# Kernel optimization log

Hardware: AMD Instinct MI355X
Metric: run time of the kernel (lower is better)

## Reference

```python
import math
import jax, jax.numpy as jnp
import numpy as np

D_MODEL = 512
N_HEADS = 8
HD = D_MODEL // N_HEADS  # 64
RATIO = 8      # csa_compress_ratio
STRIDE = 4     # csa_compress_stride
WINDOW = 128   # csa_window_size
THETA = 10000.0


def _rope_freqs(L):
    half = HD // 2
    inv_freq = 1.0 / (THETA ** (jnp.arange(half, dtype=jnp.float32) / half))
    t = jnp.arange(L, dtype=jnp.float32)
    f = t[:, None] * inv_freq[None, :]  # [L, half]
    return jnp.cos(f), jnp.sin(f)


def _apply_rope(x, cos, sin):
    # x: [B, H, L, hd]
    half = x.shape[-1] // 2
    x1, x2 = x[..., :half], x[..., half:]
    cos = cos[None, None]
    sin = sin[None, None]
    return jnp.concatenate([x1 * cos - x2 * sin, x1 * sin + x2 * cos], axis=-1)


def setup_inputs() -> dict:
    key = jax.random.key(0)
    ks = jax.random.split(key, 9)
    B, L, D = 2, 2048, D_MODEL
    s = 0.02
    return {
        "x": jax.random.normal(ks[0], (B, L, D), dtype=jnp.float32),
        "wq": jax.random.normal(ks[1], (D, D), dtype=jnp.float32) * s,
        "wk": jax.random.normal(ks[2], (D, D), dtype=jnp.float32) * s,
        "wv": jax.random.normal(ks[3], (D, D), dtype=jnp.float32) * s,
        "wo": jax.random.normal(ks[4], (D, D), dtype=jnp.float32) * s,
        "wk_c": jax.random.normal(ks[5], (D, D), dtype=jnp.float32) * s,
        "wv_c": jax.random.normal(ks[6], (D, D), dtype=jnp.float32) * s,
        "gate_logits": jax.random.normal(ks[7], (RATIO,), dtype=jnp.float32) * s,
        "sink_logit": jnp.zeros((N_HEADS, 1), dtype=jnp.float32),
    }


def reference(x, wq, wk, wv, wo, wk_c, wv_c, gate_logits, sink_logit):
    B, L, D = x.shape
    f32 = jnp.float32

    def heads(t):  # [B,L,D] -> [B,H,L,hd]
        return t.reshape(B, L, N_HEADS, HD).transpose(0, 2, 1, 3)

    q = heads(x @ wq.T)
    k = heads(x @ wk.T)
    v = heads(x @ wv.T)

    cos, sin = _rope_freqs(L)
    q = _apply_rope(q.astype(f32), cos, sin).astype(x.dtype)
    k = _apply_rope(k.astype(f32), cos, sin).astype(x.dtype)

    # --- KV compression: strided overlapping windows, learned gate pooling ---
    n_windows = max(1, (L - RATIO) // STRIDE + 1)
    idx = jnp.clip(
        jnp.arange(RATIO)[None, :] + jnp.arange(n_windows)[:, None] * STRIDE, 0, L - 1
    )  # [Lc, ratio]
    windows = x[:, idx, :]  # [B, Lc, ratio, D]
    gate_w = jax.nn.softmax(gate_logits)
    x_c = jnp.einsum("bwrd,r->bwd", windows, gate_w)  # [B, Lc, D]
    Lc = n_windows

    k_c = x_c @ wk_c.T
    v_c = x_c @ wv_c.T
    k_c = k_c.reshape(B, Lc, N_HEADS, HD).transpose(0, 2, 1, 3)
    v_c = v_c.reshape(B, Lc, N_HEADS, HD).transpose(0, 2, 1, 3)

    scale = math.sqrt(HD)
    pos = jnp.arange(L)

    # compressed branch: causal on compressed-entry end positions
    comp_scores = jnp.einsum("bhqd,bhkd->bhqk", q, k_c) / scale  # [B,H,L,Lc]
    entry_end = jnp.arange(Lc) * STRIDE + RATIO - 1
    causal_c = pos[:, None] >= entry_end[None, :]
    comp_scores = jnp.where(causal_c[None, None], comp_scores, -jnp.inf)

    # local window branch: causal band of width WINDOW
    win_scores = jnp.einsum("bhqd,bhkd->bhqk", q, k) / scale  # [B,H,L,L]
    dist = pos[:, None] - pos[None, :]
    win_mask = (dist >= 0) & (dist < WINDOW)
    win_scores = jnp.where(win_mask[None, None], win_scores, -jnp.inf)

    sink = jnp.broadcast_to(sink_logit[None, :, None, :], (B, N_HEADS, L, 1))

    all_scores = jnp.concatenate(
        [comp_scores.astype(f32), win_scores.astype(f32), sink.astype(f32)], axis=-1
    )
    attn = jax.nn.softmax(all_scores, axis=-1).astype(x.dtype)

    w_comp = attn[..., :Lc]
    w_win = attn[..., Lc:Lc + L]
    out = jnp.einsum("bhqk,bhkd->bhqd", w_comp, v_c) + jnp.einsum(
        "bhqk,bhkd->bhqd", w_win, v
    )
    out = out.transpose(0, 2, 1, 3).reshape(B, L, D)
    return out @ wo.T
```

## Files before the change

### kernel.cpp

```cpp
#include <hip/hip_runtime.h>
#include <hip/hip_bf16.h>
#include <cmath>

#define BATCH 2
#define LSEQ 2048
#define DMODEL 512
#define NHEADS 8
#define HD 64
#define RATIO 8
#define STRIDE 4
#define WINDOW 128
#define LC 511

typedef short short8 __attribute__((ext_vector_type(8)));
typedef float floatx4 __attribute__((ext_vector_type(4)));

__device__ inline unsigned short f2bf(float f) {
  unsigned u = __float_as_uint(f);
  u += 0x7FFFu + ((u >> 16) & 1u);
  return (unsigned short)(u >> 16);
}

__device__ inline void gld_lds16(const unsigned short* g, short* l) {
  __builtin_amdgcn_global_load_lds(
      (const __attribute__((address_space(1))) unsigned int*)g,
      (__attribute__((address_space(3))) unsigned int*)l, 16, 0, 0);
}

__global__ void conv_all(const float* __restrict__ x,
                         const float* __restrict__ w0, const float* __restrict__ w1,
                         const float* __restrict__ w2, const float* __restrict__ w3,
                         const float* __restrict__ w4, const float* __restrict__ w5,
                         const float* __restrict__ gate,
                         unsigned short* __restrict__ xb,
                         unsigned short* __restrict__ wqkvb,
                         unsigned short* __restrict__ wkvcb,
                         unsigned short* __restrict__ wob,
                         unsigned short* __restrict__ xcb,
                         float2* __restrict__ cstab) {
  int idx = blockIdx.x * blockDim.x + threadIdx.x;
  if (idx < 917504) {
    const float* src;
    unsigned short* dst;
    int off;
    if (idx < 524288) {
      src = x; dst = xb; off = idx;
    } else {
      int r = idx - 524288;
      int wi = r >> 16;
      off = r & 65535;
      switch (wi) {
        case 0: src = w0; dst = wqkvb; break;
        case 1: src = w1; dst = wqkvb + 4 * 65536; break;
        case 2: src = w2; dst = wqkvb + 8 * 65536; break;
        case 3: src = w3; dst = wkvcb; break;
        case 4: src = w4; dst = wkvcb + 4 * 65536; break;
        default: src = w5; dst = wob; break;
      }
    }
    float4 v = ((const float4*)src)[off];
    ushort4 o;
    o.x = f2bf(v.x); o.y = f2bf(v.y); o.z = f2bf(v.z); o.w = f2bf(v.w);
    ((ushort4*)dst)[off] = o;
  } else if (idx < 1048320) {
    int r = idx - 917504;
    int d4 = r & 127;
    int t = r >> 7;
    int w = t % LC;
    int b = t / LC;
    float g[8];
    float m = -1e30f;
#pragma unroll
    for (int i = 0; i < 8; ++i) { g[i] = gate[i]; m = fmaxf(m, g[i]); }
    float ssum = 0.f;
#pragma unroll
    for (int i = 0; i < 8; ++i) { g[i] = __expf(g[i] - m); ssum += g[i]; }
    float inv = 1.f / ssum;
    const float* xb4 = x + ((size_t)(b * LSEQ + w * STRIDE)) * DMODEL + d4 * 4;
    float4 acc = make_float4(0.f, 0.f, 0.f, 0.f);
#pragma unroll
    for (int i = 0; i < 8; ++i) {
      float4 v = *(const float4*)(xb4 + (size_t)i * DMODEL);
      acc.x += g[i] * v.x; acc.y += g[i] * v.y;
      acc.z += g[i] * v.z; acc.w += g[i] * v.w;
    }
    ushort4 o;
    o.x = f2bf(acc.x * inv); o.y = f2bf(acc.y * inv);
    o.z = f2bf(acc.z * inv); o.w = f2bf(acc.w * inv);
    ((ushort4*)xcb)[(size_t)(b * LC + w) * 128 + d4] = o;
  } else {
    int e = idx - 1048320;
    int p = e >> 5, j = e & 31;
    float inv_freq = __expf(-(float)j * (9.210340371976184f / 32.f));
    float s, c;
    sincosf((float)p * inv_freq, &s, &c);
    cstab[e] = make_float2(c, s);
  }
}

__global__ __launch_bounds__(256) void proj_gemm(
    const unsigned short* __restrict__ xb, const unsigned short* __restrict__ xcb,
    const unsigned short* __restrict__ wqkvb, const unsigned short* __restrict__ wkvcb,
    const float2* __restrict__ cstab,
    unsigned short* __restrict__ qbuf, unsigned short* __restrict__ kbuf,
    unsigned short* __restrict__ vbuf, unsigned short* __restrict__ kcb,
    unsigned short* __restrict__ vcb) {
  __shared__ short As[128 * 64];
  __shared__ short Bs[128 * 64];
  const int tid = threadIdx.x;
  const int w = tid >> 6, l = tid & 63;
  const int lr = l & 15, lg = l >> 4;

  const int bid = blockIdx.x;
  const bool qkv = (bid < 384);
  const unsigned short* Ap;
  const unsigned short* Bp;
  int bm, bn, Am1;
  if (qkv) {
    Ap = xb; Bp = wqkvb; bm = (bid & 31) * 128; bn = (bid >> 5) * 128; Am1 = 4095;
  } else {
    int r = bid - 384;
    Ap = xcb; Bp = wkvcb; bm = (r & 7) * 128; bn = (r >> 3) * 128; Am1 = 1021;
  }
  const int wm = (w >> 1) * 64, wn = (w & 1) * 64;

  floatx4 acc[4][4];
#pragma unroll
  for (int i = 0; i < 4; ++i)
#pragma unroll
    for (int j = 0; j < 4; ++j) acc[i][j] = 0.f;

  const int trow = tid >> 3;
  const int cs = (tid & 7) ^ (trow & 7);
  size_t aoffs[4];
#pragma unroll
  for (int i = 0; i < 4; ++i) {
    int ar = bm + trow + i * 32;
    if (ar > Am1) ar = Am1;
    aoffs[i] = (size_t)ar * DMODEL + cs * 8;
  }
  const size_t boff = (size_t)(bn + trow) * DMODEL + cs * 8;
  const int ldsbase = (tid & 192) * 8;

  for (int k0 = 0; k0 < DMODEL; k0 += 64) {
    __syncthreads();
#pragma unroll
    for (int i = 0; i < 4; ++i) {
      gld_lds16(Ap + aoffs[i] + k0, As + i * 2048 + ldsbase);
      gld_lds16(Bp + boff + (size_t)i * 32 * DMODEL + k0, Bs + i * 2048 + ldsbase);
    }
    __syncthreads();

#pragma unroll
    for (int kk = 0; kk < 2; ++kk) {
      const int kc16 = kk * 4 + lg;
      short8 a[4], bf[4];
#pragma unroll
      for (int mi = 0; mi < 4; ++mi) {
        int r = wm + mi * 16 + lr;
        a[mi] = *(const short8*)&As[r * 64 + ((kc16 ^ (r & 7)) * 8)];
      }
#pragma unroll
      for (int nj = 0; nj < 4; ++nj) {
        int r = wn + nj * 16 + lr;
        bf[nj] = *(const short8*)&Bs[r * 64 + ((kc16 ^ (r & 7)) * 8)];
      }
#pragma unroll
      for (int mi = 0; mi < 4; ++mi)
#pragma unroll
        for (int nj = 0; nj < 4; ++nj)
          acc[mi][nj] = __builtin_amdgcn_mfma_f32_16x16x32_bf16(
              a[mi], bf[nj], acc[mi][nj], 0, 0, 0);
    }
  }

  if (qkv) {
    if (bn < 1024) {
      unsigned short* dst = (bn < 512) ? qbuf : kbuf;
      const int cbase = (bn + wn) & 511;
#pragma unroll
      for (int mi = 0; mi < 4; ++mi) {
#pragma unroll
        for (int i = 0; i < 4; ++i) {
          int row = bm + wm + mi * 16 + lg * 4 + i;
          int p = row & 2047;
#pragma unroll
          for (int nj = 0; nj < 2; ++nj) {
            float2 cssin = cstab[p * 32 + nj * 16 + lr];
            float a = acc[mi][nj][i], b2 = acc[mi][nj + 2][i];
            int cc = cbase + nj * 16 + lr;
            dst[(size_t)row * 512 + cc] = f2bf(a * cssin.x - b2 * cssin.y);
            dst[(size_t)row * 512 + cc + 32] = f2bf(a * cssin.y + b2 * cssin.x);
          }
        }
      }
    } else {
#pragma unroll
      for (int mi = 0; mi < 4; ++mi) {
#pragma unroll
        for (int i = 0; i < 4; ++i) {
          int row = bm + wm + mi * 16 + lg * 4 + i;
#pragma unroll
          for (int nj = 0; nj < 4; ++nj) {
            int col = bn + wn + nj * 16 + lr - 1024;
            vbuf[(size_t)row * 512 + col] = f2bf(acc[mi][nj][i]);
          }
        }
      }
    }
  } else {
    unsigned short* dst = ((bn + wn) < 512) ? kcb : vcb;
    const int cbase = (bn + wn) & 511;
#pragma unroll
    for (int mi = 0; mi < 4; ++mi) {
#pragma unroll
      for (int i = 0; i < 4; ++i) {
        int row = bm + wm + mi * 16 + lg * 4 + i;
        if (row < 1022) {
#pragma unroll
          for (int nj = 0; nj < 4; ++nj)
            dst[(size_t)row * 512 + cbase + nj * 16 + lr] = f2bf(acc[mi][nj][i]);
        }
      }
    }
  }
}

__global__ __launch_bounds__(256) void wo_gemm(
    const unsigned short* __restrict__ A, const unsigned short* __restrict__ B,
    float* __restrict__ C) {
  __shared__ short As[128 * 64];
  __shared__ short Bs[64 * 64];
  const int tid = threadIdx.x;
  const int w = tid >> 6, l = tid & 63;
  const int lr = l & 15, lg = l >> 4;
  const int bm = blockIdx.x * 128, bn = blockIdx.y * 64;
  const int wm = (w >> 1) * 64, wn = (w & 1) * 32;

  floatx4 acc[4][2];
#pragma unroll
  for (int i = 0; i < 4; ++i)
#pragma unroll
    for (int j = 0; j < 2; ++j) acc[i][j] = 0.f;

  const int trow = tid >> 3;
  const int cs = (tid & 7) ^ (trow & 7);
  const size_t aoff = (size_t)(bm + trow) * DMODEL + cs * 8;
  const size_t boff = (size_t)(bn + trow) * DMODEL + cs * 8;
  const int ldsbase = (tid & 192) * 8;

  for (int k0 = 0; k0 < DMODEL; k0 += 64) {
    __syncthreads();
#pragma unroll
    for (int i = 0; i < 4; ++i)
      gld_lds16(A + aoff + (size_t)i * 32 * DMODEL + k0, As + i * 2048 + ldsbase);
#pragma unroll
    for (int i = 0; i < 2; ++i)
      gld_lds16(B + boff + (size_t)i * 32 * DMODEL + k0, Bs + i * 2048 + ldsbase);
    __syncthreads();

#pragma unroll
    for (int kk = 0; kk < 2; ++kk) {
      const int kc16 = kk * 4 + lg;
      short8 a[4], bf[2];
#pragma unroll
      for (int mi = 0; mi < 4; ++mi) {
        int r = wm + mi * 16 + lr;
        a[mi] = *(const short8*)&As[r * 64 + ((kc16 ^ (r & 7)) * 8)];
      }
#pragma unroll
      for (int nj = 0; nj < 2; ++nj) {
        int r = wn + nj * 16 + lr;
        bf[nj] = *(const short8*)&Bs[r * 64 + ((kc16 ^ (r & 7)) * 8)];
      }
#pragma unroll
      for (int mi = 0; mi < 4; ++mi)
#pragma unroll
        for (int nj = 0; nj < 2; ++nj)
          acc[mi][nj] = __builtin_amdgcn_mfma_f32_16x16x32_bf16(
              a[mi], bf[nj], acc[mi][nj], 0, 0, 0);
    }
  }

#pragma unroll
  for (int mi = 0; mi < 4; ++mi) {
#pragma unroll
    for (int i = 0; i < 4; ++i) {
      int row = bm + wm + mi * 16 + lg * 4 + i;
#pragma unroll
      for (int nj = 0; nj < 2; ++nj)
        C[(size_t)row * 512 + bn + wn + nj * 16 + lr] = acc[mi][nj][i];
    }
  }
}

__global__ __launch_bounds__(256, 2) void attn_kernel(
    const unsigned short* __restrict__ qb, const unsigned short* __restrict__ kb,
    const unsigned short* __restrict__ vb, const unsigned short* __restrict__ kcb,
    const unsigned short* __restrict__ vcb, const float* __restrict__ sink,
    unsigned short* __restrict__ ob) {
  __shared__ short Ks[2][64][72];
  __shared__ short Vt[2][64][72];
  __shared__ short Pl[4][16][72];

  const int n = blockIdx.x;
  const int b = n >> 8;
  const int mm = n & 255;
  const int h = mm >> 5;
  int qt = mm & 31;
  if (b) qt = 31 - qt;
  const int q0 = qt * 64;
  const int tid = threadIdx.x;
  const int w = tid >> 6, l = tid & 63;
  const int lr = l & 15, lg = l >> 4;
  const int hoff = h * HD;

  short8 Qa0, Qa1;
  {
    const unsigned short* qrow =
        qb + ((size_t)(b * LSEQ + q0 + w * 16 + lr)) * DMODEL + hoff;
    Qa0 = *(const short8*)(qrow + lg * 8);
    Qa1 = *(const short8*)(qrow + 32 + lg * 8);
  }

  floatx4 Oacc[4];
#pragma unroll
  for (int f = 0; f < 4; ++f) Oacc[f] = 0.f;
  float mrow = -3.0e38f, lrow = 0.f;

  int ncm = q0 / 4 + 15;
  if (ncm > LC) ncm = LC;
  const int ntc = (ncm + 63) >> 6;
  const int w0 = (q0 > 127) ? (q0 - 127) : 0;
  const int ntw = (q0 + 64 - w0 + 63) >> 6;
  const int ntt = ntc + ntw;

  const int skey = tid >> 2, sd = (tid & 3) * 16;
  const int vkey = (tid & 31) * 2, vd = (tid >> 5) * 8;
  const int p = q0 + w * 16 + lr;

  short8 kreg0, kreg1, vreg0, vreg1;

  auto load_tile = [&](int tt) {
    const bool isC = (tt < ntc);
    const int tbase = isC ? tt * 64 : (w0 + (tt - ntc) * 64);
    const unsigned short* Kp = isC ? kcb : kb;
    const unsigned short* Vp = isC ? vcb : vb;
    const int rmax = isC ? (LC - 1) : (LSEQ - 1);
    const size_t brow = isC ? (size_t)(b * LC) : (size_t)(b * LSEQ);
    int kr = tbase + skey;      if (kr > rmax) kr = rmax;
    int vr0 = tbase + vkey;     if (vr0 > rmax) vr0 = rmax;
    int vr1 = tbase + vkey + 1; if (vr1 > rmax) vr1 = rmax;
    const unsigned short* src = Kp + (brow + kr) * DMODEL + hoff + sd;
    kreg0 = *(const short8*)(src);
    kreg1 = *(const short8*)(src + 8);
    vreg0 = *(const short8*)(Vp + (brow + vr0) * DMODEL + hoff + vd);
    vreg1 = *(const short8*)(Vp + (brow + vr1) * DMODEL + hoff + vd);
  };
  auto store_tile = [&](int bsel) {
    *(short8*)&Ks[bsel][skey][sd] = kreg0;
    *(short8*)&Ks[bsel][skey][sd + 8] = kreg1;
#pragma unroll
    for (int j = 0; j < 8; ++j) {
      unsigned pk = (unsigned)(unsigned short)vreg0[j] |
                    ((unsigned)(unsigned short)vreg1[j] << 16);
      *(unsigned*)&Vt[bsel][vd + j][vkey] = pk;
    }
  };

  load_tile(0);

  for (int tt = 0; tt < ntt; ++tt) {
    const int bsel = tt & 1;
    store_tile(bsel);
    if (tt + 1 < ntt) load_tile(tt + 1);
    __syncthreads();

    const bool isC = (tt < ntc);
    const int tbase = isC ? tt * 64 : (w0 + (tt - ntc) * 64);

    floatx4 S4[4];
    __builtin_amdgcn_s_setprio(1);
#pragma unroll
    for (int f = 0; f < 4; ++f) {
      floatx4 acc = 0.f;
      short8 kf0 = *(const short8*)&Ks[bsel][f * 16 + lr][lg * 8];
      short8 kf1 = *(const short8*)&Ks[bsel][f * 16 + lr][32 + lg * 8];
      acc = __builtin_amdgcn_mfma_f32_16x16x32_bf16(kf0, Qa0, acc, 0, 0, 0);
      acc = __builtin_amdgcn_mfma_f32_16x16x32_bf16(kf1, Qa1, acc, 0, 0, 0);
      S4[f] = acc;
    }
    __builtin_amdgcn_s_setprio(0);

    float tmax = -3.0e38f;
#pragma unroll
    for (int f = 0; f < 4; ++f) {
#pragma unroll
      for (int i = 0; i < 4; ++i) {
        const int key = tbase + f * 16 + lg * 4 + i;
        bool valid;
        if (isC) valid = (key <= LC - 1) && (p >= key * 4 + 7);
        else     valid = (p >= key) && (p - key < WINDOW);
        float s = valid ? S4[f][i] * 0.125f : -3.0e38f;
        S4[f][i] = s;
        tmax = fmaxf(tmax, s);
      }
    }
    tmax = fmaxf(tmax, __shfl_xor(tmax, 16));
    tmax = fmaxf(tmax, __shfl_xor(tmax, 32));

    if (__any(tmax > mrow)) {
      float mn = fmaxf(mrow, tmax);
      float r = __expf(mrow - mn);
      mrow = mn;
      lrow *= r;
      float rb[4];
#pragma unroll
      for (int i = 0; i < 4; ++i) rb[i] = __shfl(r, lg * 4 + i);
#pragma unroll
      for (int f = 0; f < 4; ++f) {
#pragma unroll
        for (int i = 0; i < 4; ++i) Oacc[f][i] *= rb[i];
      }
    }

    float lsum = 0.f;
#pragma unroll
    for (int f = 0; f < 4; ++f) {
      float e0 = (S4[f][0] > -1.0e38f) ? __expf(S4[f][0] - mrow) : 0.f;
      float e1 = (S4[f][1] > -1.0e38f) ? __expf(S4[f][1] - mrow) : 0.f;
      float e2 = (S4[f][2] > -1.0e38f) ? __expf(S4[f][2] - mrow) : 0.f;
      float e3 = (S4[f][3] > -1.0e38f) ? __expf(S4[f][3] - mrow) : 0.f;
      lsum += (e0 + e1) + (e2 + e3);
      uint2 pk;
      pk.x = (unsigned)f2bf(e0) | ((unsigned)f2bf(e1) << 16);
      pk.y = (unsigned)f2bf(e2) | ((unsigned)f2bf(e3) << 16);
      *(uint2*)&Pl[w][lr][f * 16 + lg * 4] = pk;
    }
    lsum += __shfl_xor(lsum, 16);
    lsum += __shfl_xor(lsum, 32);
    lrow += lsum;
    asm volatile("s_waitcnt lgkmcnt(0)" ::: "memory");

    __builtin_amdgcn_s_setprio(1);
#pragma unroll
    for (int c = 0; c < 2; ++c) {
      short8 Pa = *(const short8*)&Pl[w][lr][c * 32 + lg * 8];
#pragma unroll
      for (int f = 0; f < 4; ++f) {
        short8 Vf = *(const short8*)&Vt[bsel][f * 16 + lr][c * 32 + lg * 8];
        Oacc[f] = __builtin_amdgcn_mfma_f32_16x16x32_bf16(Pa, Vf, Oacc[f], 0, 0, 0);
      }
    }
    __builtin_amdgcn_s_setprio(0);
  }

  const float snk = sink[h];
  float ms = fmaxf(mrow, snk);
  float sc = __expf(mrow - ms);
  float li = lrow * sc + __expf(snk - ms);
  float osc = sc / li;
  float ob4[4];
#pragma unroll
  for (int i = 0; i < 4; ++i) ob4[i] = __shfl(osc, lg * 4 + i);
#pragma unroll
  for (int f = 0; f < 4; ++f) {
#pragma unroll
    for (int i = 0; i < 4; ++i) {
      size_t row = (size_t)(b * LSEQ + q0 + w * 16 + lg * 4 + i);
      ob[row * DMODEL + hoff + f * 16 + lr] = f2bf(Oacc[f][i] * ob4[i]);
    }
  }
}

extern "C" void kernel_launch(void* const* d_in, const int* in_sizes, int n_in,
                              void* d_out, int out_size, void* d_ws, size_t ws_size,
                              hipStream_t stream) {
  const float* x    = (const float*)d_in[0];
  const float* wq   = (const float*)d_in[1];
  const float* wk   = (const float*)d_in[2];
  const float* wv   = (const float*)d_in[3];
  const float* wo   = (const float*)d_in[4];
  const float* wkc  = (const float*)d_in[5];
  const float* wvc  = (const float*)d_in[6];
  const float* gate = (const float*)d_in[7];
  const float* sink = (const float*)d_in[8];
  float* out = (float*)d_out;

  const int BL  = BATCH * LSEQ;
  const int BLC = BATCH * LC;
  const int NX  = BATCH * LSEQ * DMODEL;
  const int NW  = DMODEL * DMODEL;

  char* wp = (char*)d_ws;
  auto carve = [&](size_t bytes) {
    char* r = wp;
    wp += (bytes + 255) & ~(size_t)255;
    return r;
  };
  unsigned short* qbuf = (unsigned short*)carve((size_t)BL * DMODEL * 2);
  unsigned short* kbuf = (unsigned short*)carve((size_t)BL * DMODEL * 2);
  unsigned short* vbuf = (unsigned short*)carve((size_t)BL * DMODEL * 2);
  unsigned short* kcb  = (unsigned short*)carve((size_t)BLC * DMODEL * 2);
  unsigned short* vcb  = (unsigned short*)carve((size_t)BLC * DMODEL * 2);
  unsigned short* xb   = (unsigned short*)carve((size_t)NX * 2);
  unsigned short* xcb  = (unsigned short*)carve((size_t)BLC * DMODEL * 2);
  unsigned short* ob   = (unsigned short*)carve((size_t)BL * DMODEL * 2);
  unsigned short* wqkvb = (unsigned short*)carve((size_t)NW * 3 * 2);
  unsigned short* wkvcb = (unsigned short*)carve((size_t)NW * 2 * 2);
  unsigned short* wob   = (unsigned short*)carve((size_t)NW * 2);
  float2* cstab = (float2*)carve((size_t)2048 * 32 * sizeof(float2));

  conv_all<<<4351, 256, 0, stream>>>(x, wq, wk, wv, wkc, wvc, wo, gate,
                                     xb, wqkvb, wkvcb, wob, xcb, cstab);

  proj_gemm<<<448, 256, 0, stream>>>(xb, xcb, wqkvb, wkvcb, cstab,
                                     qbuf, kbuf, vbuf, kcb, vcb);

  attn_kernel<<<BATCH * NHEADS * (LSEQ / 64), 256, 0, stream>>>(
      qbuf, kbuf, vbuf, kcb, vcb, sink, ob);

  wo_gemm<<<dim3(BL / 128, DMODEL / 64), 256, 0, stream>>>(ob, wob, out);
}
```

Before: 59.73 us.

## Double-buffer GEMM LDS tiles and skip fully-masked attention tiles per wave

The projection and output GEMMs now use two LDS buffers. The next K-slice's global-to-LDS load is issued before the current slice's MFMAs, so there is one barrier per iteration instead of two. In the attention kernel, each wave skips the compute for key tiles that are fully masked for its 16 query rows. For tiles that are fully valid it uses a mask-free scaling path, cutting wasted MFMA and masking work. Doubling LDS per block (64KB in proj_gemm) may lower occupancy. Skipping compute per wave relies on no barrier following the compute inside the loop.

```diff
diff --git a/kernel.cpp b/kernel.cpp
--- a/kernel.cpp
+++ b/kernel.cpp
@@ -105,8 +105,8 @@
     unsigned short* __restrict__ qbuf, unsigned short* __restrict__ kbuf,
     unsigned short* __restrict__ vbuf, unsigned short* __restrict__ kcb,
     unsigned short* __restrict__ vcb) {
-  __shared__ short As[128 * 64];
-  __shared__ short Bs[128 * 64];
+  __shared__ short As[2][128 * 64];
+  __shared__ short Bs[2][128 * 64];
   const int tid = threadIdx.x;
   const int w = tid >> 6, l = tid & 63;
   const int lr = l & 15, lg = l >> 4;
@@ -142,15 +142,20 @@
   const size_t boff = (size_t)(bn + trow) * DMODEL + cs * 8;
   const int ldsbase = (tid & 192) * 8;
 
-  for (int k0 = 0; k0 < DMODEL; k0 += 64) {
-    __syncthreads();
+  auto stage = [&](int ks, int buf) {
+    const int k0 = ks * 64;
 #pragma unroll
     for (int i = 0; i < 4; ++i) {
-      gld_lds16(Ap + aoffs[i] + k0, As + i * 2048 + ldsbase);
-      gld_lds16(Bp + boff + (size_t)i * 32 * DMODEL + k0, Bs + i * 2048 + ldsbase);
-    }
-    __syncthreads();
-
+      gld_lds16(Ap + aoffs[i] + k0, &As[buf][i * 2048 + ldsbase]);
+      gld_lds16(Bp + boff + (size_t)i * 32 * DMODEL + k0, &Bs[buf][i * 2048 + ldsbase]);
+    }
+  };
+
+  stage(0, 0);
+  __syncthreads();
+  for (int ks = 0; ks < 8; ++ks) {
+    const int cur = ks & 1;
+    if (ks < 7) stage(ks + 1, cur ^ 1);
 #pragma unroll
     for (int kk = 0; kk < 2; ++kk) {
       const int kc16 = kk * 4 + lg;
@@ -158,12 +163,12 @@
 #pragma unroll
       for (int mi = 0; mi < 4; ++mi) {
         int r = wm + mi * 16 + lr;
-        a[mi] = *(const short8*)&As[r * 64 + ((kc16 ^ (r & 7)) * 8)];
+        a[mi] = *(const short8*)&As[cur][r * 64 + ((kc16 ^ (r & 7)) * 8)];
       }
 #pragma unroll
       for (int nj = 0; nj < 4; ++nj) {
         int r = wn + nj * 16 + lr;
-        bf[nj] = *(const short8*)&Bs[r * 64 + ((kc16 ^ (r & 7)) * 8)];
+        bf[nj] = *(const short8*)&Bs[cur][r * 64 + ((kc16 ^ (r & 7)) * 8)];
       }
 #pragma unroll
       for (int mi = 0; mi < 4; ++mi)
@@ -172,6 +177,7 @@
           acc[mi][nj] = __builtin_amdgcn_mfma_f32_16x16x32_bf16(
               a[mi], bf[nj], acc[mi][nj], 0, 0, 0);
     }
+    __syncthreads();
   }
 
   if (qkv) {
@@ -229,8 +235,8 @@
 __global__ __launch_bounds__(256) void wo_gemm(
     const unsigned short* __restrict__ A, const unsigned short* __restrict__ B,
     float* __restrict__ C) {
-  __shared__ short As[128 * 64];
-  __shared__ short Bs[64 * 64];
+  __shared__ short As[2][128 * 64];
+  __shared__ short Bs[2][64 * 64];
   const int tid = threadIdx.x;
   const int w = tid >> 6, l = tid & 63;
   const int lr = l & 15, lg = l >> 4;
@@ -249,16 +255,21 @@
   const size_t boff = (size_t)(bn + trow) * DMODEL + cs * 8;
   const int ldsbase = (tid & 192) * 8;
 
-  for (int k0 = 0; k0 < DMODEL; k0 += 64) {
-    __syncthreads();
+  auto stage = [&](int ks, int buf) {
+    const int k0 = ks * 64;
 #pragma unroll
     for (int i = 0; i < 4; ++i)
-      gld_lds16(A + aoff + (size_t)i * 32 * DMODEL + k0, As + i * 2048 + ldsbase);
+      gld_lds16(A + aoff + (size_t)i * 32 * DMODEL + k0, &As[buf][i * 2048 + ldsbase]);
 #pragma unroll
     for (int i = 0; i < 2; ++i)
-      gld_lds16(B + boff + (size_t)i * 32 * DMODEL + k0, Bs + i * 2048 + ldsbase);
-    __syncthreads();
-
+      gld_lds16(B + boff + (size_t)i * 32 * DMODEL + k0, &Bs[buf][i * 2048 + ldsbase]);
+  };
+
+  stage(0, 0);
+  __syncthreads();
+  for (int ks = 0; ks < 8; ++ks) {
+    const int cur = ks & 1;
+    if (ks < 7) stage(ks + 1, cur ^ 1);
 #pragma unroll
     for (int kk = 0; kk < 2; ++kk) {
       const int kc16 = kk * 4 + lg;
@@ -266,12 +277,12 @@
 #pragma unroll
       for (int mi = 0; mi < 4; ++mi) {
         int r = wm + mi * 16 + lr;
-        a[mi] = *(const short8*)&As[r * 64 + ((kc16 ^ (r & 7)) * 8)];
+        a[mi] = *(const short8*)&As[cur][r * 64 + ((kc16 ^ (r & 7)) * 8)];
       }
 #pragma unroll
       for (int nj = 0; nj < 2; ++nj) {
         int r = wn + nj * 16 + lr;
-        bf[nj] = *(const short8*)&Bs[r * 64 + ((kc16 ^ (r & 7)) * 8)];
+        bf[nj] = *(const short8*)&Bs[cur][r * 64 + ((kc16 ^ (r & 7)) * 8)];
       }
 #pragma unroll
       for (int mi = 0; mi < 4; ++mi)
@@ -280,6 +291,7 @@
           acc[mi][nj] = __builtin_amdgcn_mfma_f32_16x16x32_bf16(
               a[mi], bf[nj], acc[mi][nj], 0, 0, 0);
     }
+    __syncthreads();
   }
 
 #pragma unroll
@@ -338,6 +350,7 @@
   const int skey = tid >> 2, sd = (tid & 3) * 16;
   const int vkey = (tid & 31) * 2, vd = (tid >> 5) * 8;
   const int p = q0 + w * 16 + lr;
+  const int pmin = q0 + w * 16;
 
   short8 kreg0, kreg1, vreg0, vreg1;
 
@@ -379,6 +392,13 @@
     const bool isC = (tt < ntc);
     const int tbase = isC ? tt * 64 : (w0 + (tt - ntc) * 64);
 
+    const bool deadTile = isC ? (tbase * 4 + 7 > pmin + 15)
+                              : (tbase > pmin + 15);
+    if (deadTile) continue;
+    const bool fullTile = isC
+        ? ((tbase + 63) * 4 + 7 <= pmin) && (tbase + 63 <= LC - 1)
+        : (tbase + 63 <= pmin) && (tbase >= pmin + 15 - (WINDOW - 1));
+
     floatx4 S4[4];
     __builtin_amdgcn_s_setprio(1);
 #pragma unroll
@@ -393,17 +413,29 @@
     __builtin_amdgcn_s_setprio(0);
 
     float tmax = -3.0e38f;
-#pragma unroll
-    for (int f = 0; f < 4; ++f) {
-#pragma unroll
-      for (int i = 0; i < 4; ++i) {
-        const int key = tbase + f * 16 + lg * 4 + i;
-        bool valid;
-        if (isC) valid = (key <= LC - 1) && (p >= key * 4 + 7);
-        else     valid = (p >= key) && (p - key < WINDOW);
-        float s = valid ? S4[f][i] * 0.125f : -3.0e38f;
-        S4[f][i] = s;
-        tmax = fmaxf(tmax, s);
+    if (fullTile) {
+#pragma unroll
+      for (int f = 0; f < 4; ++f) {
+#pragma unroll
+        for (int i = 0; i < 4; ++i) {
+          float s = S4[f][i] * 0.125f;
+          S4[f][i] = s;
+          tmax = fmaxf(tmax, s);
+        }
+      }
+    } else {
+#pragma unroll
+      for (int f = 0; f < 4; ++f) {
+#pragma unroll
+        for (int i = 0; i < 4; ++i) {
+          const int key = tbase + f * 16 + lg * 4 + i;
+          bool valid;
+          if (isC) valid = (key <= LC - 1) && (p >= key * 4 + 7);
+          else     valid = (p >= key) && (p - key < WINDOW);
+          float s = valid ? S4[f][i] * 0.125f : -3.0e38f;
+          S4[f][i] = s;
+          tmax = fmaxf(tmax, s);
+        }
       }
     }
     tmax = fmaxf(tmax, __shfl_xor(tmax, 16));
```

Measured after the change: 56.01 us (median of 2 runs). 6.2% less time.
